# Optimization experiments

Measured on AMD Instinct MI355X. Metric: run time of the kernel, lower is better.

## Reference

```python
import jax, jax.numpy as jnp
import numpy as np

N = 100000          # nodes
E = 3200000         # edges
F_IN = 128          # num_node_features
C = 32              # num_candidate_node_types


def _gcn_conv(x, src, dst, W, b, n_nodes):
    """PyG GCNConv: add self loops, symmetric deg^-1/2 normalization, then linear."""
    h = x @ W  # [N, out]
    # degree on A + I (edge weight 1), counted on target nodes
    deg = jnp.zeros((n_nodes,), h.dtype).at[dst].add(1.0) + 1.0
    dinv = jax.lax.rsqrt(deg)  # deg >= 1 so safe
    norm = dinv[src] * dinv[dst]            # [E]
    msg = h[src] * norm[:, None]            # gather + scale, [E, out]
    out = jax.ops.segment_sum(msg, dst, num_segments=n_nodes)
    out = out + h * (dinv * dinv)[:, None]  # self-loop contribution
    return out + b


def _relu6(x):
    return jnp.clip(x, 0.0, 6.0)


def setup_inputs() -> dict:
    key = jax.random.key(0)
    ks = jax.random.split(key, 16)
    def lin(k, fan_in, fan_out):
        lim = 1.0 / np.sqrt(fan_in)
        kw, kb = jax.random.split(k)
        W = jax.random.uniform(kw, (fan_in, fan_out), jnp.float32, -lim, lim)
        b = jax.random.uniform(kb, (fan_out,), jnp.float32, -lim, lim)
        return W, b
    W1, b1 = lin(ks[0], F_IN, 16)
    W2, b2 = lin(ks[1], 16, 24)
    W3, b3 = lin(ks[2], 24, 32)
    Ws1, bs1 = lin(ks[3], 32, 16)
    Ws2, bs2 = lin(ks[4], 16, C)
    We1, be1 = lin(ks[5], 32, 24)
    We2, be2 = lin(ks[6], 24, C)
    x = jax.random.normal(ks[7], (N, F_IN), jnp.float32)
    edge_index = jax.random.randint(ks[8], (2, E), 0, N, jnp.int64)
    candidate_set = jax.random.randint(ks[9], (C,), 0, C, jnp.int64)
    return dict(x=x, edge_index=edge_index, candidate_set=candidate_set,
                W1=W1, b1=b1, W2=W2, b2=b2, W3=W3, b3=b3,
                Ws1=Ws1, bs1=bs1, Ws2=Ws2, bs2=bs2,
                We1=We1, be1=be1, We2=We2, be2=be2)


def reference(x, edge_index, candidate_set,
              W1, b1, W2, b2, W3, b3,
              Ws1, bs1, Ws2, bs2, We1, be1, We2, be2):
    src, dst = edge_index[0], edge_index[1]
    h = _gcn_conv(x, src, dst, W1, b1, N)   # [N, 16] (no activation in source)
    h = _gcn_conv(h, src, dst, W2, b2, N)   # [N, 24]
    h = _gcn_conv(h, src, dst, W3, b3, N)   # [N, 32]
    # start-node head: Linear -> ReLU6 -> Linear -> Softmax, then Categorical sample
    s_logits = _relu6(h @ Ws1 + bs1) @ Ws2 + bs2         # [N, C]
    k1, k2 = jax.random.split(jax.random.key(42))
    start_node = jax.random.categorical(k1, s_logits, axis=-1)  # [N] ints in [0, C)
    # gather rows at sampled indices and append (vectorized form of the source's cat)
    combined = jnp.concatenate([h, h[start_node]], axis=0)      # [2N, 32]
    e_logits = _relu6(combined @ We1 + be1) @ We2 + be2          # [2N, C]
    end_node = jax.random.categorical(k2, e_logits, axis=-1)    # [2N]
    return start_node, end_node
```

## Files before the change

### kernel.cpp

```cpp
#include <hip/hip_runtime.h>
#include <hip/hip_bf16.h>
#include <math.h>

#define TPB 256
#define BSHIFT 8
#define BRANGE (1 << BSHIFT)
#define CHUNK 8192
#define MAXB 512

__host__ __device__ inline void tf2x32(unsigned ks0, unsigned ks1,
                                       unsigned x0, unsigned x1,
                                       unsigned& o0, unsigned& o1) {
  const unsigned ks2 = ks0 ^ ks1 ^ 0x1BD11BDAu;
  unsigned v0 = x0 + ks0, v1 = x1 + ks1;
#define TF_RND(r) { v0 += v1; v1 = (v1 << (r)) | (v1 >> (32 - (r))); v1 ^= v0; }
  TF_RND(13) TF_RND(15) TF_RND(26) TF_RND(6)
  v0 += ks1; v1 += ks2 + 1u;
  TF_RND(17) TF_RND(29) TF_RND(16) TF_RND(24)
  v0 += ks2; v1 += ks0 + 2u;
  TF_RND(13) TF_RND(15) TF_RND(26) TF_RND(6)
  v0 += ks0; v1 += ks1 + 3u;
  TF_RND(17) TF_RND(29) TF_RND(16) TF_RND(24)
  v0 += ks1; v1 += ks2 + 4u;
  TF_RND(13) TF_RND(15) TF_RND(26) TF_RND(6)
  v0 += ks2; v1 += ks0 + 5u;
#undef TF_RND
  o0 = v0; o1 = v1;
}

__device__ __forceinline__ unsigned bits32(unsigned k0, unsigned k1, unsigned idx) {
  unsigned o0, o1;
  tf2x32(k0, k1, 0u, idx, o0, o1);
  return o0 ^ o1;
}

__device__ __forceinline__ float bits_to_u(unsigned bits) {
  float f = __uint_as_float((bits >> 9) | 0x3f800000u) - 1.0f;
  return (f > 0.0f) ? f : 1.17549435e-38f;
}

__device__ __forceinline__ float gumbel_exact(unsigned k0, unsigned k1, unsigned idx) {
  float u = bits_to_u(bits32(k0, k1, idx));
  float w = (float)(-log((double)u));
  return (float)(-log((double)w));
}

__device__ __forceinline__ float gumbel_fast(unsigned k0, unsigned k1, unsigned idx) {
  float u = bits_to_u(bits32(k0, k1, idx));
  float w = -logf(u);
  return -logf(w);
}

__global__ void hist_kernel(const int* __restrict__ dst, int* __restrict__ histT,
                            int E, int nblk, int nbuckets) {
  __shared__ int hist[MAXB];
  for (int i = threadIdx.x; i < nbuckets; i += TPB) hist[i] = 0;
  __syncthreads();
  int beg = blockIdx.x * CHUNK;
  int end = min(beg + CHUNK, E);
  for (int e = beg + threadIdx.x; e < end; e += TPB)
    atomicAdd(&hist[dst[e] >> BSHIFT], 1);
  __syncthreads();
  for (int i = threadIdx.x; i < nbuckets; i += TPB)
    histT[(size_t)i * nblk + blockIdx.x] = hist[i];
}

__global__ void colscan_kernel(int* __restrict__ histT, int* __restrict__ btot, int nblk) {
  __shared__ int sh[MAXB];
  int b = blockIdx.x;
  int t = threadIdx.x;
  sh[t] = (t < nblk) ? histT[(size_t)b * nblk + t] : 0;
  __syncthreads();
  for (int ofs = 1; ofs < MAXB; ofs <<= 1) {
    int v = (t >= ofs) ? sh[t - ofs] : 0;
    __syncthreads();
    sh[t] += v;
    __syncthreads();
  }
  if (t < nblk) histT[(size_t)b * nblk + t] = (t == 0) ? 0 : sh[t - 1];
  if (t == MAXB - 1) btot[b] = sh[MAXB - 1];
}

__global__ void bucketscan_kernel(const int* __restrict__ btot, int* __restrict__ bbase,
                                  int nbuckets, int E) {
  __shared__ int sh[MAXB];
  int t = threadIdx.x;
  sh[t] = (t < nbuckets) ? btot[t] : 0;
  __syncthreads();
  for (int ofs = 1; ofs < MAXB; ofs <<= 1) {
    int v = (t >= ofs) ? sh[t - ofs] : 0;
    __syncthreads();
    sh[t] += v;
    __syncthreads();
  }
  if (t < nbuckets) bbase[t] = (t == 0) ? 0 : sh[t - 1];
  if (t == 0) bbase[nbuckets] = E;
}

__global__ void place_kernel(const int* __restrict__ src, const int* __restrict__ dst,
                             const int* __restrict__ histT, const int* __restrict__ bbase,
                             unsigned* __restrict__ packed, int E, int nblk, int nbuckets) {
  __shared__ int cur[MAXB];
  for (int i = threadIdx.x; i < nbuckets; i += TPB)
    cur[i] = histT[(size_t)i * nblk + blockIdx.x] + bbase[i];
  __syncthreads();
  int beg = blockIdx.x * CHUNK;
  int end = min(beg + CHUNK, E);
  for (int e = beg + threadIdx.x; e < end; e += TPB) {
    int s = src[e], d = dst[e];
    int b = d >> BSHIFT;
    int pos = atomicAdd(&cur[b], 1);
    packed[pos] = (unsigned)s | ((unsigned)(d & (BRANGE - 1)) << 20);
  }
}

__global__ void bucket_place_kernel(const int* __restrict__ bbase,
                                    const unsigned* __restrict__ packed,
                                    int* __restrict__ csr_src, int* __restrict__ rowptr,
                                    float* __restrict__ dinv, float* __restrict__ dinv2,
                                    int N, int nbuckets) {
  __shared__ int cnt[BRANGE];
  __shared__ int sh[BRANGE];
  __shared__ int cur[BRANGE];
  int b = blockIdx.x;
  int base = b << BSHIFT;
  int range_n = min(BRANGE, N - base);
  int t = threadIdx.x;
  cnt[t] = 0;
  __syncthreads();
  int beg = bbase[b], end = bbase[b + 1];
  for (int e = beg + t; e < end; e += TPB)
    atomicAdd(&cnt[packed[e] >> 20], 1);
  __syncthreads();
  sh[t] = cnt[t];
  __syncthreads();
  for (int ofs = 1; ofs < BRANGE; ofs <<= 1) {
    int v = (t >= ofs) ? sh[t - ofs] : 0;
    __syncthreads();
    sh[t] += v;
    __syncthreads();
  }
  int excl = (t == 0) ? 0 : sh[t - 1];
  cur[t] = beg + excl;
  if (t < range_n) {
    rowptr[base + t] = beg + excl;
    float d = (float)(cnt[t] + 1);
    float di = 1.0f / sqrtf(d);
    dinv[base + t] = di;
    dinv2[base + t] = di * di;
  }
  if (b == nbuckets - 1 && t == 0) rowptr[N] = end;
  __syncthreads();
  for (int e = beg + t; e < end; e += TPB) {
    unsigned p = packed[e];
    int dstoff = (int)(p >> 20);
    int s = (int)(p & 0xFFFFFu);
    int pos = atomicAdd(&cur[dstoff], 1);
    csr_src[pos] = s;
  }
}

template <int K, int J>
__global__ void matmul_kernel(const float* __restrict__ A, const float* __restrict__ W,
                              float* __restrict__ out, int N) {
  int t = blockIdx.x * blockDim.x + threadIdx.x;
  if (t >= N * J) return;
  int n = t / J, j = t % J;
  const float* a = A + (size_t)n * K;
  double acc = 0.0;
  for (int k = 0; k < K; ++k) acc += (double)a[k] * (double)W[k * J + j];
  out[(size_t)n * J + j] = (float)acc;
}

template <int J>
__global__ void gather_shfl_kernel(const int* __restrict__ rowptr,
                                   const int* __restrict__ csr_src,
                                   const float* __restrict__ dinv,
                                   const float* __restrict__ h,
                                   const float* __restrict__ dinv2,
                                   const float* __restrict__ b,
                                   float* __restrict__ out, int N) {
  int t = blockIdx.x * blockDim.x + threadIdx.x;
  int n = t / J, j = t % J;
  if (n >= N) return;
  int beg = rowptr[n], end = rowptr[n + 1];
  float dn = dinv[n];
  double acc = 0.0;
  for (int i = beg; i < end; i += J) {
    int m = end - i; if (m > J) m = J;
    int idx = i + j; if (idx >= end) idx = end - 1;
    int   sj = csr_src[idx];
    float wj = dinv[sj];
    int k = 0;
    for (; k + 8 <= m; k += 8) {
      int s0 = __shfl(sj, k + 0, J), s1 = __shfl(sj, k + 1, J);
      int s2 = __shfl(sj, k + 2, J), s3 = __shfl(sj, k + 3, J);
      int s4 = __shfl(sj, k + 4, J), s5 = __shfl(sj, k + 5, J);
      int s6 = __shfl(sj, k + 6, J), s7 = __shfl(sj, k + 7, J);
      float w0 = __shfl(wj, k + 0, J) * dn, w1 = __shfl(wj, k + 1, J) * dn;
      float w2 = __shfl(wj, k + 2, J) * dn, w3 = __shfl(wj, k + 3, J) * dn;
      float w4 = __shfl(wj, k + 4, J) * dn, w5 = __shfl(wj, k + 5, J) * dn;
      float w6 = __shfl(wj, k + 6, J) * dn, w7 = __shfl(wj, k + 7, J) * dn;
      float g0 = h[(size_t)s0 * J + j], g1 = h[(size_t)s1 * J + j];
      float g2 = h[(size_t)s2 * J + j], g3 = h[(size_t)s3 * J + j];
      float g4 = h[(size_t)s4 * J + j], g5 = h[(size_t)s5 * J + j];
      float g6 = h[(size_t)s6 * J + j], g7 = h[(size_t)s7 * J + j];
      acc += (double)g0 * (double)w0;
      acc += (double)g1 * (double)w1;
      acc += (double)g2 * (double)w2;
      acc += (double)g3 * (double)w3;
      acc += (double)g4 * (double)w4;
      acc += (double)g5 * (double)w5;
      acc += (double)g6 * (double)w6;
      acc += (double)g7 * (double)w7;
    }
    for (; k < m; ++k) {
      int   s = __shfl(sj, k, J);
      float w = __shfl(wj, k, J) * dn;
      acc += (double)h[(size_t)s * J + j] * (double)w;
    }
  }
  acc += (double)h[(size_t)n * J + j] * (double)dinv2[n];
  out[(size_t)n * J + j] = (float)acc + b[j];
}

template <int J>
__global__ void gather_agg_kernel(const int* __restrict__ rowptr,
                                  const int* __restrict__ csr_src,
                                  const float* __restrict__ dinv,
                                  const float* __restrict__ h,
                                  const float* __restrict__ dinv2,
                                  const float* __restrict__ b,
                                  float* __restrict__ out, int N) {
  int t = blockIdx.x * blockDim.x + threadIdx.x;
  int n = t / J, j = t % J;
  if (n >= N) return;
  int beg = rowptr[n], end = rowptr[n + 1];
  float dn = dinv[n];
  double acc = 0.0;
  int i = beg;
  for (; i + 8 <= end; i += 8) {
    int s0 = csr_src[i + 0], s1 = csr_src[i + 1], s2 = csr_src[i + 2], s3 = csr_src[i + 3];
    int s4 = csr_src[i + 4], s5 = csr_src[i + 5], s6 = csr_src[i + 6], s7 = csr_src[i + 7];
    float g0 = h[(size_t)s0 * J + j], g1 = h[(size_t)s1 * J + j];
    float g2 = h[(size_t)s2 * J + j], g3 = h[(size_t)s3 * J + j];
    float g4 = h[(size_t)s4 * J + j], g5 = h[(size_t)s5 * J + j];
    float g6 = h[(size_t)s6 * J + j], g7 = h[(size_t)s7 * J + j];
    float w0 = dinv[s0] * dn, w1 = dinv[s1] * dn, w2 = dinv[s2] * dn, w3 = dinv[s3] * dn;
    float w4 = dinv[s4] * dn, w5 = dinv[s5] * dn, w6 = dinv[s6] * dn, w7 = dinv[s7] * dn;
    acc += (double)g0 * (double)w0;
    acc += (double)g1 * (double)w1;
    acc += (double)g2 * (double)w2;
    acc += (double)g3 * (double)w3;
    acc += (double)g4 * (double)w4;
    acc += (double)g5 * (double)w5;
    acc += (double)g6 * (double)w6;
    acc += (double)g7 * (double)w7;
  }
  for (; i < end; ++i) {
    int s = csr_src[i];
    float w = dinv[s] * dn;
    acc += (double)h[(size_t)s * J + j] * (double)w;
  }
  acc += (double)h[(size_t)n * J + j] * (double)dinv2[n];
  out[(size_t)n * J + j] = (float)acc + b[j];
}

__global__ void hid_start_kernel(const float* __restrict__ h,
                                 const float* __restrict__ Ws1, const float* __restrict__ bs1,
                                 float* __restrict__ hid, int N) {
  int t = blockIdx.x * blockDim.x + threadIdx.x;
  if (t >= N * 16) return;
  int n = t / 16, j = t % 16;
  const float* hr = h + (size_t)n * 32;
  double a = 0.0;
#pragma unroll
  for (int k = 0; k < 32; ++k) a += (double)hr[k] * (double)Ws1[k * 16 + j];
  float v = (float)a + bs1[j];
  hid[t] = fminf(fmaxf(v, 0.0f), 6.0f);
}

__global__ void hid_end_kernel(const float* __restrict__ h, const int* __restrict__ start,
                               const float* __restrict__ We1, const float* __restrict__ be1,
                               float* __restrict__ hid, int N) {
  int t = blockIdx.x * blockDim.x + threadIdx.x;
  if (t >= 2 * N * 24) return;
  int r = t / 24, j = t % 24;
  int row = (r < N) ? r : start[r - N];
  const float* hr = h + (size_t)row * 32;
  double a = 0.0;
#pragma unroll
  for (int k = 0; k < 32; ++k) a += (double)hr[k] * (double)We1[k * 24 + j];
  float v = (float)a + be1[j];
  hid[t] = fminf(fmaxf(v, 0.0f), 6.0f);
}

template <int K>
__global__ void pick_kernel(const float* __restrict__ hid,
                            const float* __restrict__ W2, const float* __restrict__ b2,
                            int* __restrict__ outw, int R, unsigned k0, unsigned k1) {
  int t = blockIdx.x * blockDim.x + threadIdx.x;
  int r = t >> 5;
  int c = t & 31;
  if (r >= R) return;
  const float* hr = hid + (size_t)r * K;

  float af = 0.0f;
#pragma unroll
  for (int k = 0; k < K; ++k) af = fmaf(hr[k], W2[k * 32 + c], af);
  float zf = af + b2[c] + gumbel_fast(k0, k1, (unsigned)(r * 32 + c));

  float m1 = zf; int i1 = c; float m2 = -INFINITY;
#pragma unroll
  for (int m = 16; m >= 1; m >>= 1) {
    float om1 = __shfl_xor(m1, m, 32);
    int   oi1 = __shfl_xor(i1, m, 32);
    float om2 = __shfl_xor(m2, m, 32);
    if (om1 > m1 || (om1 == m1 && oi1 < i1)) {
      m2 = fmaxf(m1, om2);
      m1 = om1; i1 = oi1;
    } else {
      m2 = fmaxf(m2, om1);
    }
  }

  if (m1 - m2 >= 1e-3f) {
    if (c == 0) outw[r] = i1;
    return;
  }

  double a = 0.0;
#pragma unroll
  for (int k = 0; k < K; ++k) a += (double)hr[k] * (double)W2[k * 32 + c];
  float logit = (float)a + b2[c];
  float z = logit + gumbel_exact(k0, k1, (unsigned)(r * 32 + c));
  int best = c;
#pragma unroll
  for (int m = 16; m >= 1; m >>= 1) {
    float oz = __shfl_xor(z, m, 32);
    int   ob = __shfl_xor(best, m, 32);
    if (oz > z || (oz == z && ob < best)) { z = oz; best = ob; }
  }
  if (c == 0) outw[r] = best;
}

extern "C" void kernel_launch(void* const* d_in, const int* in_sizes, int n_in,
                              void* d_out, int out_size, void* d_ws, size_t ws_size,
                              hipStream_t stream) {
  const float* x   = (const float*)d_in[0];
  const int*   ei  = (const int*)d_in[1];
  const float* W1  = (const float*)d_in[3];
  const float* b1  = (const float*)d_in[4];
  const float* W2  = (const float*)d_in[5];
  const float* b2  = (const float*)d_in[6];
  const float* W3  = (const float*)d_in[7];
  const float* b3  = (const float*)d_in[8];
  const float* Ws1 = (const float*)d_in[9];
  const float* bs1 = (const float*)d_in[10];
  const float* Ws2 = (const float*)d_in[11];
  const float* bs2 = (const float*)d_in[12];
  const float* We1 = (const float*)d_in[13];
  const float* be1 = (const float*)d_in[14];
  const float* We2 = (const float*)d_in[15];
  const float* be2 = (const float*)d_in[16];

  const int N = in_sizes[0] / 128;
  const int E = in_sizes[1] / 2;
  const int* srcv = ei;
  const int* dstv = ei + E;
  const int nbuckets = (N + BRANGE - 1) >> BSHIFT;
  const int nblk = (E + CHUNK - 1) / CHUNK;

  char* ws = (char*)d_ws;
  size_t off = 0;
  float*    hA      = (float*)(ws + off);    off += (size_t)N * 32 * 4;
  float*    hB      = (float*)(ws + off);    off += (size_t)N * 32 * 4;
  int*      csr_src = (int*)(ws + off);      off += (size_t)E * 4;
  unsigned* packed  = (unsigned*)(ws + off); off += (size_t)E * 4;
  float*    dinv    = (float*)(ws + off);    off += (size_t)N * 4;
  float*    dinv2   = (float*)(ws + off);    off += (size_t)N * 4;
  int*      rowptr  = (int*)(ws + off);      off += (size_t)(N + 1) * 4;
  int*      histT   = (int*)(ws + off);      off += (size_t)nbuckets * nblk * 4;
  int*      btot    = (int*)(ws + off);      off += (size_t)MAXB * 4;
  int*      bbase   = (int*)(ws + off);      off += (size_t)(MAXB + 1) * 4;
  float* hid_start = hA;
  float* hid_end   = (float*)csr_src;

  unsigned k1a, k1b, k2a, k2b;
  tf2x32(0u, 42u, 0u, 0u, k1a, k1b);
  tf2x32(0u, 42u, 0u, 1u, k2a, k2b);

  hist_kernel<<<nblk, TPB, 0, stream>>>(dstv, histT, E, nblk, nbuckets);
  colscan_kernel<<<nbuckets, MAXB, 0, stream>>>(histT, btot, nblk);
  bucketscan_kernel<<<1, MAXB, 0, stream>>>(btot, bbase, nbuckets, E);
  place_kernel<<<nblk, TPB, 0, stream>>>(srcv, dstv, histT, bbase, packed, E, nblk, nbuckets);
  bucket_place_kernel<<<nbuckets, TPB, 0, stream>>>(bbase, packed, csr_src, rowptr,
                                                    dinv, dinv2, N, nbuckets);

  matmul_kernel<128, 16><<<((size_t)N * 16 + TPB - 1) / TPB, TPB, 0, stream>>>(x, W1, hA, N);
  gather_shfl_kernel<16><<<((size_t)N * 16 + TPB - 1) / TPB, TPB, 0, stream>>>(
      rowptr, csr_src, dinv, hA, dinv2, b1, hB, N);

  matmul_kernel<16, 24><<<((size_t)N * 24 + TPB - 1) / TPB, TPB, 0, stream>>>(hB, W2, hA, N);
  gather_agg_kernel<24><<<((size_t)N * 24 + TPB - 1) / TPB, TPB, 0, stream>>>(
      rowptr, csr_src, dinv, hA, dinv2, b2, hB, N);

  matmul_kernel<24, 32><<<((size_t)N * 32 + TPB - 1) / TPB, TPB, 0, stream>>>(hB, W3, hA, N);
  gather_shfl_kernel<32><<<((size_t)N * 32 + TPB - 1) / TPB, TPB, 0, stream>>>(
      rowptr, csr_src, dinv, hA, dinv2, b3, hB, N);

  int* outI = (int*)d_out;

  hid_start_kernel<<<((size_t)N * 16 + TPB - 1) / TPB, TPB, 0, stream>>>(hB, Ws1, bs1, hid_start, N);
  pick_kernel<16><<<((size_t)N * 32 + TPB - 1) / TPB, TPB, 0, stream>>>(
      hid_start, Ws2, bs2, outI, N, k1a, k1b);

  hid_end_kernel<<<((size_t)2 * N * 24 + TPB - 1) / TPB, TPB, 0, stream>>>(hB, outI, We1, be1, hid_end, N);
  pick_kernel<24><<<((size_t)2 * N * 32 + TPB - 1) / TPB, TPB, 0, stream>>>(
      hid_end, We2, be2, outI + N, 2 * N, k2a, k2b);
}
```

Measured before the change: 559.0 us.

## Pad layer-2 features to stride 32 and gather two floats per lane

The layer-2 linear output is now written with a padded row stride of 32 so rows are aligned for float2 access. Layers 2 and 3 aggregate with a new 16-lane shuffle kernel in which each lane loads a float2 and keeps two double accumulators, and neighbor indices and weights are broadcast with shuffles. This replaces the scalar gather_agg kernel for layer 2 and the 32-wide shuffle kernel for layer 3, cutting threads, shuffles and load instructions per edge. For the 24-wide layer, 4 of the 16 lanes do redundant clamped work and the padded buffer costs extra memory footprint.

Measured after the change: 560.6 us. No clear change (+0.3%).

```diff
diff --git a/kernel.cpp b/kernel.cpp
--- a/kernel.cpp
+++ b/kernel.cpp
@@ -160,7 +160,7 @@
   }
 }
 
-template <int K, int J>
+template <int K, int J, int LDO>
 __global__ void matmul_kernel(const float* __restrict__ A, const float* __restrict__ W,
                               float* __restrict__ out, int N) {
   int t = blockIdx.x * blockDim.x + threadIdx.x;
@@ -169,7 +169,7 @@
   const float* a = A + (size_t)n * K;
   double acc = 0.0;
   for (int k = 0; k < K; ++k) acc += (double)a[k] * (double)W[k * J + j];
-  out[(size_t)n * J + j] = (float)acc;
+  out[(size_t)n * LDO + j] = (float)acc;
 }
 
 template <int J>
@@ -224,46 +224,74 @@
   out[(size_t)n * J + j] = (float)acc + b[j];
 }
 
-template <int J>
-__global__ void gather_agg_kernel(const int* __restrict__ rowptr,
-                                  const int* __restrict__ csr_src,
-                                  const float* __restrict__ dinv,
-                                  const float* __restrict__ h,
-                                  const float* __restrict__ dinv2,
-                                  const float* __restrict__ b,
-                                  float* __restrict__ out, int N) {
-  int t = blockIdx.x * blockDim.x + threadIdx.x;
-  int n = t / J, j = t % J;
+template <int JA, int W, int LDH>
+__global__ void gather_shfl2_kernel(const int* __restrict__ rowptr,
+                                    const int* __restrict__ csr_src,
+                                    const float* __restrict__ dinv,
+                                    const float* __restrict__ h,
+                                    const float* __restrict__ dinv2,
+                                    const float* __restrict__ b,
+                                    float* __restrict__ out, int N) {
+  int t = blockIdx.x * blockDim.x + threadIdx.x;
+  int n = t / W, j = t % W;
   if (n >= N) return;
+  const int NJ = JA / 2;
+  int jj = (j < NJ) ? j : (NJ - 1);
   int beg = rowptr[n], end = rowptr[n + 1];
   float dn = dinv[n];
-  double acc = 0.0;
-  int i = beg;
-  for (; i + 8 <= end; i += 8) {
-    int s0 = csr_src[i + 0], s1 = csr_src[i + 1], s2 = csr_src[i + 2], s3 = csr_src[i + 3];
-    int s4 = csr_src[i + 4], s5 = csr_src[i + 5], s6 = csr_src[i + 6], s7 = csr_src[i + 7];
-    float g0 = h[(size_t)s0 * J + j], g1 = h[(size_t)s1 * J + j];
-    float g2 = h[(size_t)s2 * J + j], g3 = h[(size_t)s3 * J + j];
-    float g4 = h[(size_t)s4 * J + j], g5 = h[(size_t)s5 * J + j];
-    float g6 = h[(size_t)s6 * J + j], g7 = h[(size_t)s7 * J + j];
-    float w0 = dinv[s0] * dn, w1 = dinv[s1] * dn, w2 = dinv[s2] * dn, w3 = dinv[s3] * dn;
-    float w4 = dinv[s4] * dn, w5 = dinv[s5] * dn, w6 = dinv[s6] * dn, w7 = dinv[s7] * dn;
-    acc += (double)g0 * (double)w0;
-    acc += (double)g1 * (double)w1;
-    acc += (double)g2 * (double)w2;
-    acc += (double)g3 * (double)w3;
-    acc += (double)g4 * (double)w4;
-    acc += (double)g5 * (double)w5;
-    acc += (double)g6 * (double)w6;
-    acc += (double)g7 * (double)w7;
-  }
-  for (; i < end; ++i) {
-    int s = csr_src[i];
-    float w = dinv[s] * dn;
-    acc += (double)h[(size_t)s * J + j] * (double)w;
-  }
-  acc += (double)h[(size_t)n * J + j] * (double)dinv2[n];
-  out[(size_t)n * J + j] = (float)acc + b[j];
+  double acc0 = 0.0, acc1 = 0.0;
+  for (int i = beg; i < end; i += W) {
+    int m = end - i; if (m > W) m = W;
+    int idx = i + j; if (idx >= end) idx = end - 1;
+    int   sj = csr_src[idx];
+    float wj = dinv[sj];
+    int k = 0;
+    for (; k + 8 <= m; k += 8) {
+      int s0 = __shfl(sj, k + 0, W), s1 = __shfl(sj, k + 1, W);
+      int s2 = __shfl(sj, k + 2, W), s3 = __shfl(sj, k + 3, W);
+      int s4 = __shfl(sj, k + 4, W), s5 = __shfl(sj, k + 5, W);
+      int s6 = __shfl(sj, k + 6, W), s7 = __shfl(sj, k + 7, W);
+      float w0 = __shfl(wj, k + 0, W) * dn, w1 = __shfl(wj, k + 1, W) * dn;
+      float w2 = __shfl(wj, k + 2, W) * dn, w3 = __shfl(wj, k + 3, W) * dn;
+      float w4 = __shfl(wj, k + 4, W) * dn, w5 = __shfl(wj, k + 5, W) * dn;
+      float w6 = __shfl(wj, k + 6, W) * dn, w7 = __shfl(wj, k + 7, W) * dn;
+      float2 g0 = *(const float2*)&h[(size_t)s0 * LDH + 2 * jj];
+      float2 g1 = *(const float2*)&h[(size_t)s1 * LDH + 2 * jj];
+      float2 g2 = *(const float2*)&h[(size_t)s2 * LDH + 2 * jj];
+      float2 g3 = *(const float2*)&h[(size_t)s3 * LDH + 2 * jj];
+      float2 g4 = *(const float2*)&h[(size_t)s4 * LDH + 2 * jj];
+      float2 g5 = *(const float2*)&h[(size_t)s5 * LDH + 2 * jj];
+      float2 g6 = *(const float2*)&h[(size_t)s6 * LDH + 2 * jj];
+      float2 g7 = *(const float2*)&h[(size_t)s7 * LDH + 2 * jj];
+      acc0 += (double)g0.x * (double)w0; acc1 += (double)g0.y * (double)w0;
+      acc0 += (double)g1.x * (double)w1; acc1 += (double)g1.y * (double)w1;
+      acc0 += (double)g2.x * (double)w2; acc1 += (double)g2.y * (double)w2;
+      acc0 += (double)g3.x * (double)w3; acc1 += (double)g3.y * (double)w3;
+      acc0 += (double)g4.x * (double)w4; acc1 += (double)g4.y * (double)w4;
+      acc0 += (double)g5.x * (double)w5; acc1 += (double)g5.y * (double)w5;
+      acc0 += (double)g6.x * (double)w6; acc1 += (double)g6.y * (double)w6;
+      acc0 += (double)g7.x * (double)w7; acc1 += (double)g7.y * (double)w7;
+    }
+    for (; k < m; ++k) {
+      int   s = __shfl(sj, k, W);
+      float w = __shfl(wj, k, W) * dn;
+      float2 g = *(const float2*)&h[(size_t)s * LDH + 2 * jj];
+      acc0 += (double)g.x * (double)w;
+      acc1 += (double)g.y * (double)w;
+    }
+  }
+  {
+    float2 gs = *(const float2*)&h[(size_t)n * LDH + 2 * jj];
+    double d2 = (double)dinv2[n];
+    acc0 += (double)gs.x * d2;
+    acc1 += (double)gs.y * d2;
+  }
+  if (j < NJ) {
+    float2 o;
+    o.x = (float)acc0 + b[2 * j];
+    o.y = (float)acc1 + b[2 * j + 1];
+    *(float2*)&out[(size_t)n * JA + 2 * j] = o;
+  }
 }
 
 __global__ void hid_start_kernel(const float* __restrict__ h,
@@ -397,16 +425,16 @@
   bucket_place_kernel<<<nbuckets, TPB, 0, stream>>>(bbase, packed, csr_src, rowptr,
                                                     dinv, dinv2, N, nbuckets);
 
-  matmul_kernel<128, 16><<<((size_t)N * 16 + TPB - 1) / TPB, TPB, 0, stream>>>(x, W1, hA, N);
+  matmul_kernel<128, 16, 16><<<((size_t)N * 16 + TPB - 1) / TPB, TPB, 0, stream>>>(x, W1, hA, N);
   gather_shfl_kernel<16><<<((size_t)N * 16 + TPB - 1) / TPB, TPB, 0, stream>>>(
       rowptr, csr_src, dinv, hA, dinv2, b1, hB, N);
 
-  matmul_kernel<16, 24><<<((size_t)N * 24 + TPB - 1) / TPB, TPB, 0, stream>>>(hB, W2, hA, N);
-  gather_agg_kernel<24><<<((size_t)N * 24 + TPB - 1) / TPB, TPB, 0, stream>>>(
+  matmul_kernel<16, 24, 32><<<((size_t)N * 24 + TPB - 1) / TPB, TPB, 0, stream>>>(hB, W2, hA, N);
+  gather_shfl2_kernel<24, 16, 32><<<((size_t)N * 16 + TPB - 1) / TPB, TPB, 0, stream>>>(
       rowptr, csr_src, dinv, hA, dinv2, b2, hB, N);
 
-  matmul_kernel<24, 32><<<((size_t)N * 32 + TPB - 1) / TPB, TPB, 0, stream>>>(hB, W3, hA, N);
-  gather_shfl_kernel<32><<<((size_t)N * 32 + TPB - 1) / TPB, TPB, 0, stream>>>(
+  matmul_kernel<24, 32, 32><<<((size_t)N * 32 + TPB - 1) / TPB, TPB, 0, stream>>>(hB, W3, hA, N);
+  gather_shfl2_kernel<32, 16, 32><<<((size_t)N * 16 + TPB - 1) / TPB, TPB, 0, stream>>>(
       rowptr, csr_src, dinv, hA, dinv2, b3, hB, N);
 
   int* outI = (int*)d_out;
```
